# Optimization experiments

Measured on AMD Instinct MI355X. Metric: run time of the kernel, lower is better.

The kernel has to match this reference:

```python
import jax, jax.numpy as jnp
import numpy as np

B, N, DIN, DOUT, H = 4, 2048, 256, 256, 4
HD = DOUT // H
NEG_SLOPE = 0.2


def setup_inputs() -> dict:
    key = jax.random.key(0)
    k1, k2, k3, k4, k5 = jax.random.split(key, 5)
    x = jax.random.normal(k1, (B, N, DIN), dtype=jnp.float32)
    adj = jax.random.randint(k2, (B, N, N), 0, 2).astype(jnp.float32)
    # ensure self-loops so every softmax row has at least one valid entry
    adj = jnp.maximum(adj, jnp.eye(N, dtype=jnp.float32)[None])
    # xavier-uniform-ish scales
    w_bound = float(np.sqrt(6.0 / (DIN + DOUT)))
    a_bound = float(np.sqrt(6.0 / (1 + HD)))
    W = jax.random.uniform(k3, (DOUT, DIN), jnp.float32, -w_bound, w_bound)
    a_src = jax.random.uniform(k4, (H, HD), jnp.float32, -a_bound, a_bound)
    a_dst = jax.random.uniform(k5, (H, HD), jnp.float32, -a_bound, a_bound)
    return {"x": x, "adj": adj, "W": W, "a_src": a_src, "a_dst": a_dst}


def reference(x, adj, W, a_src, a_dst):
    b, n, _ = x.shape
    h = (x @ W.T).reshape(b, n, H, HD)                      # [B,N,H,HD]
    s_src = jnp.einsum('bnhd,hd->bnh', h, a_src)            # [B,N,H]
    s_dst = jnp.einsum('bnhd,hd->bnh', h, a_dst)            # [B,N,H]
    # e[b,i,j,h] = leaky_relu(s_src[b,i,h] + s_dst[b,j,h])
    e = jax.nn.leaky_relu(s_src[:, :, None, :] + s_dst[:, None, :, :], NEG_SLOPE)
    e = jnp.where(adj[..., None] == 0, -jnp.inf, e)         # [B,N,N,H]
    alpha = jax.nn.softmax(e, axis=2)                       # softmax over j (dropout is identity at eval)
    out = jnp.einsum('bijh,bjhd->bihd', alpha, h)           # weighted aggregate
    return out.reshape(b, n, DOUT)
```

## Files before the change

### kernel.cpp

```cpp
#include <hip/hip_runtime.h>
#include <math.h>

#define Bb   4
#define Nn   2048
#define Dd   256
#define Hh   4
#define HDd  64
#define BN   (Bb * Nn)

typedef float v4f __attribute__((ext_vector_type(4)));
typedef short v8s __attribute__((ext_vector_type(8)));

__device__ __forceinline__ unsigned rne_bf16(float f) {
    unsigned u = __float_as_uint(f);
    u += 0x7fffu + ((u >> 16) & 1u);
    return u >> 16;
}

__global__ __launch_bounds__(256, 2) void k_gemm(const float* __restrict__ x,
                                                 const float* __restrict__ W,
                                                 const float* __restrict__ a_src,
                                                 const float* __restrict__ a_dst,
                                                 unsigned short* __restrict__ hbf,
                                                 float* __restrict__ ssrc,
                                                 float* __restrict__ sdst) {
    __shared__ __align__(16) unsigned short xs[2][64 * 72];
    __shared__ __align__(16) unsigned short wsm[2][64 * 72];
    __shared__ float asd[128];

    const int tid = threadIdx.x;
    const int m0 = (int)(blockIdx.x >> 2) * 64;
    const int head = (int)blockIdx.x & 3;
    const int n0 = head * 64;
    const int b = m0 >> 11;
    const int i0loc = m0 & 2047;

    if (tid < 128) {
        int sel = tid >> 6, d = tid & 63;
        asd[tid] = sel ? a_dst[n0 + d] : a_src[n0 + d];
    }

    const int wv = tid >> 6, ln = tid & 63, l15 = ln & 15, l4 = ln >> 4;
    const int mh = wv >> 1, nh = wv & 1;
    const int srow = tid >> 2, kq = (tid & 3) * 16;

    v4f acc[2][2];
#pragma unroll
    for (int g = 0; g < 2; ++g)
#pragma unroll
        for (int t = 0; t < 2; ++t) acc[g][t] = (v4f){0.f, 0.f, 0.f, 0.f};

    for (int st = 0; st < 4; ++st) {
        const int k0 = st * 64;
        __syncthreads();
        {
            float xf[16], wf[16];
            const float* xp = x + (size_t)(m0 + srow) * Dd + k0 + kq;
            const float* wp = W + (size_t)(n0 + srow) * Dd + k0 + kq;
#pragma unroll
            for (int q = 0; q < 4; ++q) {
                *(float4*)&xf[q * 4] = *(const float4*)(xp + q * 4);
                *(float4*)&wf[q * 4] = *(const float4*)(wp + q * 4);
            }
            unsigned xh[8], xl[8], wh[8], wl[8];
#pragma unroll
            for (int j = 0; j < 8; ++j) {
                unsigned h0 = rne_bf16(xf[2 * j]), h1 = rne_bf16(xf[2 * j + 1]);
                float l0 = xf[2 * j] - __uint_as_float(h0 << 16);
                float l1 = xf[2 * j + 1] - __uint_as_float(h1 << 16);
                xh[j] = h0 | (h1 << 16);
                xl[j] = rne_bf16(l0) | (rne_bf16(l1) << 16);
                unsigned g0 = rne_bf16(wf[2 * j]), g1 = rne_bf16(wf[2 * j + 1]);
                float m0f = wf[2 * j] - __uint_as_float(g0 << 16);
                float m1f = wf[2 * j + 1] - __uint_as_float(g1 << 16);
                wh[j] = g0 | (g1 << 16);
                wl[j] = rne_bf16(m0f) | (rne_bf16(m1f) << 16);
            }
            *(uint4*)(xs[0] + srow * 72 + kq)     = make_uint4(xh[0], xh[1], xh[2], xh[3]);
            *(uint4*)(xs[0] + srow * 72 + kq + 8) = make_uint4(xh[4], xh[5], xh[6], xh[7]);
            *(uint4*)(xs[1] + srow * 72 + kq)     = make_uint4(xl[0], xl[1], xl[2], xl[3]);
            *(uint4*)(xs[1] + srow * 72 + kq + 8) = make_uint4(xl[4], xl[5], xl[6], xl[7]);
            *(uint4*)(wsm[0] + srow * 72 + kq)     = make_uint4(wh[0], wh[1], wh[2], wh[3]);
            *(uint4*)(wsm[0] + srow * 72 + kq + 8) = make_uint4(wh[4], wh[5], wh[6], wh[7]);
            *(uint4*)(wsm[1] + srow * 72 + kq)     = make_uint4(wl[0], wl[1], wl[2], wl[3]);
            *(uint4*)(wsm[1] + srow * 72 + kq + 8) = make_uint4(wl[4], wl[5], wl[6], wl[7]);
        }
        __syncthreads();
        {
            v8s ah[2][2], al[2][2], bh_[2][2], bl_[2][2];
#pragma unroll
            for (int g = 0; g < 2; ++g)
#pragma unroll
                for (int kh = 0; kh < 2; ++kh) {
                    int ro = (mh * 32 + g * 16 + l15) * 72 + kh * 32 + l4 * 8;
                    ah[g][kh] = *(const v8s*)(xs[0] + ro);
                    al[g][kh] = *(const v8s*)(xs[1] + ro);
                }
#pragma unroll
            for (int t = 0; t < 2; ++t)
#pragma unroll
                for (int kh = 0; kh < 2; ++kh) {
                    int ro = (nh * 32 + t * 16 + l15) * 72 + kh * 32 + l4 * 8;
                    bh_[t][kh] = *(const v8s*)(wsm[0] + ro);
                    bl_[t][kh] = *(const v8s*)(wsm[1] + ro);
                }
#pragma unroll
            for (int g = 0; g < 2; ++g)
#pragma unroll
                for (int t = 0; t < 2; ++t)
#pragma unroll
                    for (int kh = 0; kh < 2; ++kh) {
                        acc[g][t] = __builtin_amdgcn_mfma_f32_16x16x32_bf16(ah[g][kh], bh_[t][kh], acc[g][t], 0, 0, 0);
                        acc[g][t] = __builtin_amdgcn_mfma_f32_16x16x32_bf16(al[g][kh], bh_[t][kh], acc[g][t], 0, 0, 0);
                        acc[g][t] = __builtin_amdgcn_mfma_f32_16x16x32_bf16(ah[g][kh], bl_[t][kh], acc[g][t], 0, 0, 0);
                    }
        }
    }

    __syncthreads();
    float* T = (float*)&xs[0][0];
#pragma unroll
    for (int g = 0; g < 2; ++g)
#pragma unroll
        for (int t = 0; t < 2; ++t)
#pragma unroll
            for (int r = 0; r < 4; ++r) {
                int d = nh * 32 + t * 16 + l15;
                int m = mh * 32 + g * 16 + l4 * 4 + r;
                T[d * 67 + m] = acc[g][t][r];
            }
    __syncthreads();
    if (tid < 128) {
        int m = tid & 63, sel = tid >> 6;
        float s = 0.f;
#pragma unroll
        for (int d = 0; d < 64; ++d) s += T[d * 67 + m] * asd[sel * 64 + d];
        (sel ? sdst : ssrc)[(size_t)head * BN + (size_t)b * Nn + i0loc + m] = s;
        int dloc = tid >> 1, jh = tid & 1;
        const float* row = T + dloc * 67 + jh * 32;
        unsigned pk[16];
#pragma unroll
        for (int jj = 0; jj < 16; ++jj)
            pk[jj] = rne_bf16(row[jj * 2]) | (rne_bf16(row[jj * 2 + 1]) << 16);
        unsigned short* dst = hbf +
            ((size_t)((b * 64 + (i0loc >> 5) + jh) * 256 + head * HDd + dloc)) * 32;
        uint4* d4 = (uint4*)dst;
        d4[0] = make_uint4(pk[0], pk[1], pk[2], pk[3]);
        d4[1] = make_uint4(pk[4], pk[5], pk[6], pk[7]);
        d4[2] = make_uint4(pk[8], pk[9], pk[10], pk[11]);
        d4[3] = make_uint4(pk[12], pk[13], pk[14], pk[15]);
    }
}

__global__ __launch_bounds__(512, 4) void k_aggr(const unsigned short* __restrict__ hbf,
                                                 const float* __restrict__ adj,
                                                 const float* __restrict__ ssrc,
                                                 const float* __restrict__ sdst,
                                                 float* __restrict__ out) {
    __shared__ __align__(16) unsigned short Aw[2][64 * 72];

    const int tid = threadIdx.x;
    const int bid = (int)blockIdx.x;
    const int hp  = (bid >> 3) & 1;
    const int lin = (bid & 7) | ((bid >> 4) << 3);
    const int b  = lin >> 6;
    const int i0 = (lin & 63) * 32;

    const int gi = tid >> 4, jq = tid & 15;
    const int wv = tid >> 6;
    const int hl = wv >> 2, tl = wv & 3;
    const int ln = tid & 63, l15 = ln & 15, l4 = ln >> 4;

    const float ss0 = ssrc[(size_t)(hp * 2 + 0) * BN + (size_t)b * Nn + i0 + gi];
    const float ss1 = ssrc[(size_t)(hp * 2 + 1) * BN + (size_t)b * Nn + i0 + gi];
    const float* adjr = adj + (size_t)b * Nn * Nn + (size_t)(i0 + gi) * Nn;
    const float* sdr0 = sdst + (size_t)(hp * 2 + 0) * BN + (size_t)b * Nn;
    const float* sdr1 = sdst + (size_t)(hp * 2 + 1) * BN + (size_t)b * Nn;

    const unsigned short* hrow = hbf +
        ((size_t)b * 64 * 256 + (size_t)(hp * 128 + hl * 64 + tl * 16 + l15)) * 32 + l4 * 8;

    const v8s ones = {0x3F80, 0x3F80, 0x3F80, 0x3F80, 0x3F80, 0x3F80, 0x3F80, 0x3F80};

    v4f acc[2], zac[2];
#pragma unroll
    for (int g = 0; g < 2; ++g) {
        acc[g] = (v4f){0.f, 0.f, 0.f, 0.f};
        zac[g] = (v4f){0.f, 0.f, 0.f, 0.f};
    }

    float4 ajv = *(const float4*)(adjr + jq * 4);
    float4 sda = *(const float4*)(sdr0 + jq * 4);
    float4 sdb = *(const float4*)(sdr1 + jq * 4);

    for (int st = 0; st < 32; ++st) {
        {
            const float adjv[4] = {ajv.x, ajv.y, ajv.z, ajv.w};
            const float sa[4] = {sda.x, sda.y, sda.z, sda.w};
            const float sb[4] = {sdb.x, sdb.y, sdb.z, sdb.w};
            unsigned pk0[2], pk1[2];
#pragma unroll
            for (int k = 0; k < 4; ++k) {
                float e0 = ss0 + sa[k];
                float e1 = ss1 + sb[k];
                e0 = fmaxf(e0, 0.2f * e0);
                e1 = fmaxf(e1, 0.2f * e1);
                unsigned u0 = rne_bf16(adjv[k] * __expf(e0));
                unsigned u1 = rne_bf16(adjv[k] * __expf(e1));
                if (k & 1) { pk0[k >> 1] |= u0 << 16; pk1[k >> 1] |= u1 << 16; }
                else       { pk0[k >> 1] = u0;        pk1[k >> 1] = u1; }
            }
            *(uint2*)(Aw[st & 1] + gi * 72 + jq * 4)        = make_uint2(pk0[0], pk0[1]);
            *(uint2*)(Aw[st & 1] + (32 + gi) * 72 + jq * 4) = make_uint2(pk1[0], pk1[1]);
        }
        __syncthreads();
        {
            const int jn = ((st + 1) & 31) * 64;
            ajv = *(const float4*)(adjr + jn + jq * 4);
            sda = *(const float4*)(sdr0 + jn + jq * 4);
            sdb = *(const float4*)(sdr1 + jn + jq * 4);
        }
        {
            const unsigned short* awp = Aw[st & 1];
            v8s b0 = *(const v8s*)(hrow + (size_t)(2 * st + 0) * 8192);
            v8s b1 = *(const v8s*)(hrow + (size_t)(2 * st + 1) * 8192);
            v8s a00 = *(const v8s*)(awp + (hl * 32 + l15) * 72 + l4 * 8);
            v8s a01 = *(const v8s*)(awp + (hl * 32 + l15) * 72 + 32 + l4 * 8);
            v8s a10 = *(const v8s*)(awp + (hl * 32 + 16 + l15) * 72 + l4 * 8);
            v8s a11 = *(const v8s*)(awp + (hl * 32 + 16 + l15) * 72 + 32 + l4 * 8);
            acc[0] = __builtin_amdgcn_mfma_f32_16x16x32_bf16(a00, b0, acc[0], 0, 0, 0);
            acc[0] = __builtin_amdgcn_mfma_f32_16x16x32_bf16(a01, b1, acc[0], 0, 0, 0);
            acc[1] = __builtin_amdgcn_mfma_f32_16x16x32_bf16(a10, b0, acc[1], 0, 0, 0);
            acc[1] = __builtin_amdgcn_mfma_f32_16x16x32_bf16(a11, b1, acc[1], 0, 0, 0);
            zac[0] = __builtin_amdgcn_mfma_f32_16x16x32_bf16(a00, ones, zac[0], 0, 0, 0);
            zac[0] = __builtin_amdgcn_mfma_f32_16x16x32_bf16(a01, ones, zac[0], 0, 0, 0);
            zac[1] = __builtin_amdgcn_mfma_f32_16x16x32_bf16(a10, ones, zac[1], 0, 0, 0);
            zac[1] = __builtin_amdgcn_mfma_f32_16x16x32_bf16(a11, ones, zac[1], 0, 0, 0);
        }
    }

    const int head = hp * 2 + hl;
    const int d = head * HDd + tl * 16 + l15;
#pragma unroll
    for (int g = 0; g < 2; ++g)
#pragma unroll
        for (int r = 0; r < 4; ++r) {
            float zinv = 1.f / zac[g][r];
            int i = i0 + g * 16 + l4 * 4 + r;
            out[((size_t)b * Nn + i) * Dd + d] = acc[g][r] * zinv;
        }
}

extern "C" void kernel_launch(void* const* d_in, const int* in_sizes, int n_in,
                              void* d_out, int out_size, void* d_ws, size_t ws_size,
                              hipStream_t stream) {
    const float* x     = (const float*)d_in[0];
    const float* adj   = (const float*)d_in[1];
    const float* W     = (const float*)d_in[2];
    const float* a_src = (const float*)d_in[3];
    const float* a_dst = (const float*)d_in[4];
    float* out = (float*)d_out;

    unsigned short* hbf = (unsigned short*)d_ws;
    float* ssrc = (float*)(hbf + (size_t)Bb * Nn * Dd);
    float* sdst = ssrc + (size_t)Hh * BN;

    k_gemm<<<dim3(512), dim3(256), 0, stream>>>(x, W, a_src, a_dst, hbf, ssrc, sdst);
    k_aggr<<<dim3(512), dim3(512), 0, stream>>>(hbf, adj, ssrc, sdst, out);
}
```

Before: 154.2 us.

## Generate attention weights directly in MFMA A-fragment registers, drop LDS staging

The aggregation kernel no longer writes bf16 attention weights to shared memory and synchronizes each step. Each wave instead computes its own A fragment in registers from adj/sdst loads laid out to match the MFMA operand, and covers a full head (four 16-column tiles) for 16 rows. Loads are double-buffered by hand across steps, and the block shrinks to 256 threads. This removes the LDS round trip and the barriers. In exchange, adj rows are read by both head waves, so exp work is duplicated per head pair and register pressure goes up.

```diff
diff --git a/kernel.cpp b/kernel.cpp
--- a/kernel.cpp
+++ b/kernel.cpp
@@ -152,13 +152,11 @@
     }
 }
 
-__global__ __launch_bounds__(512, 4) void k_aggr(const unsigned short* __restrict__ hbf,
+__global__ __launch_bounds__(256, 2) void k_aggr(const unsigned short* __restrict__ hbf,
                                                  const float* __restrict__ adj,
                                                  const float* __restrict__ ssrc,
                                                  const float* __restrict__ sdst,
                                                  float* __restrict__ out) {
-    __shared__ __align__(16) unsigned short Aw[2][64 * 72];
-
     const int tid = threadIdx.x;
     const int bid = (int)blockIdx.x;
     const int hp  = (bid >> 3) & 1;
@@ -166,89 +164,112 @@
     const int b  = lin >> 6;
     const int i0 = (lin & 63) * 32;
 
-    const int gi = tid >> 4, jq = tid & 15;
     const int wv = tid >> 6;
-    const int hl = wv >> 2, tl = wv & 3;
+    const int h  = hp * 2 + (wv >> 1);
+    const int isub = wv & 1;
     const int ln = tid & 63, l15 = ln & 15, l4 = ln >> 4;
 
-    const float ss0 = ssrc[(size_t)(hp * 2 + 0) * BN + (size_t)b * Nn + i0 + gi];
-    const float ss1 = ssrc[(size_t)(hp * 2 + 1) * BN + (size_t)b * Nn + i0 + gi];
-    const float* adjr = adj + (size_t)b * Nn * Nn + (size_t)(i0 + gi) * Nn;
-    const float* sdr0 = sdst + (size_t)(hp * 2 + 0) * BN + (size_t)b * Nn;
-    const float* sdr1 = sdst + (size_t)(hp * 2 + 1) * BN + (size_t)b * Nn;
-
-    const unsigned short* hrow = hbf +
-        ((size_t)b * 64 * 256 + (size_t)(hp * 128 + hl * 64 + tl * 16 + l15)) * 32 + l4 * 8;
+    const int irow = i0 + isub * 16 + l15;
+    const float ss = ssrc[(size_t)h * BN + (size_t)b * Nn + irow];
+    const float* adjr = adj  + ((size_t)b * Nn + irow) * Nn + l4 * 8;
+    const float* sdr  = sdst + (size_t)h * BN + (size_t)b * Nn + l4 * 8;
+    const unsigned short* hb0 = hbf +
+        ((size_t)b * 64 * 256 + (size_t)(h * HDd + l15)) * 32 + l4 * 8;
 
     const v8s ones = {0x3F80, 0x3F80, 0x3F80, 0x3F80, 0x3F80, 0x3F80, 0x3F80, 0x3F80};
 
-    v4f acc[2], zac[2];
-#pragma unroll
-    for (int g = 0; g < 2; ++g) {
-        acc[g] = (v4f){0.f, 0.f, 0.f, 0.f};
-        zac[g] = (v4f){0.f, 0.f, 0.f, 0.f};
-    }
-
-    float4 ajv = *(const float4*)(adjr + jq * 4);
-    float4 sda = *(const float4*)(sdr0 + jq * 4);
-    float4 sdb = *(const float4*)(sdr1 + jq * 4);
-
-    for (int st = 0; st < 32; ++st) {
-        {
-            const float adjv[4] = {ajv.x, ajv.y, ajv.z, ajv.w};
-            const float sa[4] = {sda.x, sda.y, sda.z, sda.w};
-            const float sb[4] = {sdb.x, sdb.y, sdb.z, sdb.w};
-            unsigned pk0[2], pk1[2];
-#pragma unroll
-            for (int k = 0; k < 4; ++k) {
-                float e0 = ss0 + sa[k];
-                float e1 = ss1 + sb[k];
-                e0 = fmaxf(e0, 0.2f * e0);
-                e1 = fmaxf(e1, 0.2f * e1);
-                unsigned u0 = rne_bf16(adjv[k] * __expf(e0));
-                unsigned u1 = rne_bf16(adjv[k] * __expf(e1));
-                if (k & 1) { pk0[k >> 1] |= u0 << 16; pk1[k >> 1] |= u1 << 16; }
-                else       { pk0[k >> 1] = u0;        pk1[k >> 1] = u1; }
-            }
-            *(uint2*)(Aw[st & 1] + gi * 72 + jq * 4)        = make_uint2(pk0[0], pk0[1]);
-            *(uint2*)(Aw[st & 1] + (32 + gi) * 72 + jq * 4) = make_uint2(pk1[0], pk1[1]);
-        }
-        __syncthreads();
-        {
-            const int jn = ((st + 1) & 31) * 64;
-            ajv = *(const float4*)(adjr + jn + jq * 4);
-            sda = *(const float4*)(sdr0 + jn + jq * 4);
-            sdb = *(const float4*)(sdr1 + jn + jq * 4);
-        }
-        {
-            const unsigned short* awp = Aw[st & 1];
-            v8s b0 = *(const v8s*)(hrow + (size_t)(2 * st + 0) * 8192);
-            v8s b1 = *(const v8s*)(hrow + (size_t)(2 * st + 1) * 8192);
-            v8s a00 = *(const v8s*)(awp + (hl * 32 + l15) * 72 + l4 * 8);
-            v8s a01 = *(const v8s*)(awp + (hl * 32 + l15) * 72 + 32 + l4 * 8);
-            v8s a10 = *(const v8s*)(awp + (hl * 32 + 16 + l15) * 72 + l4 * 8);
-            v8s a11 = *(const v8s*)(awp + (hl * 32 + 16 + l15) * 72 + 32 + l4 * 8);
-            acc[0] = __builtin_amdgcn_mfma_f32_16x16x32_bf16(a00, b0, acc[0], 0, 0, 0);
-            acc[0] = __builtin_amdgcn_mfma_f32_16x16x32_bf16(a01, b1, acc[0], 0, 0, 0);
-            acc[1] = __builtin_amdgcn_mfma_f32_16x16x32_bf16(a10, b0, acc[1], 0, 0, 0);
-            acc[1] = __builtin_amdgcn_mfma_f32_16x16x32_bf16(a11, b1, acc[1], 0, 0, 0);
-            zac[0] = __builtin_amdgcn_mfma_f32_16x16x32_bf16(a00, ones, zac[0], 0, 0, 0);
-            zac[0] = __builtin_amdgcn_mfma_f32_16x16x32_bf16(a01, ones, zac[0], 0, 0, 0);
-            zac[1] = __builtin_amdgcn_mfma_f32_16x16x32_bf16(a10, ones, zac[1], 0, 0, 0);
-            zac[1] = __builtin_amdgcn_mfma_f32_16x16x32_bf16(a11, ones, zac[1], 0, 0, 0);
-        }
-    }
-
-    const int head = hp * 2 + hl;
-    const int d = head * HDd + tl * 16 + l15;
-#pragma unroll
-    for (int g = 0; g < 2; ++g)
-#pragma unroll
-        for (int r = 0; r < 4; ++r) {
-            float zinv = 1.f / zac[g][r];
-            int i = i0 + g * 16 + l4 * 4 + r;
-            out[((size_t)b * Nn + i) * Dd + d] = acc[g][r] * zinv;
-        }
+    v4f acc[4], zac;
+#pragma unroll
+    for (int t = 0; t < 4; ++t) acc[t] = (v4f){0.f, 0.f, 0.f, 0.f};
+    zac = (v4f){0.f, 0.f, 0.f, 0.f};
+
+    v8s bA[8], bB[8];
+    float4 ajA[4], sdA[4], ajB[4], sdB[4];
+
+#define LOADS(stn, bb, aj_, sd_) do {                                         \
+        const int js_ = (stn) & 31;                                           \
+        const float* ap_ = adjr + js_ * 64;                                   \
+        aj_[0] = *(const float4*)(ap_ + 0);                                   \
+        aj_[1] = *(const float4*)(ap_ + 4);                                   \
+        aj_[2] = *(const float4*)(ap_ + 32);                                  \
+        aj_[3] = *(const float4*)(ap_ + 36);                                  \
+        const float* sp_ = sdr + js_ * 64;                                    \
+        sd_[0] = *(const float4*)(sp_ + 0);                                   \
+        sd_[1] = *(const float4*)(sp_ + 4);                                   \
+        sd_[2] = *(const float4*)(sp_ + 32);                                  \
+        sd_[3] = *(const float4*)(sp_ + 36);                                  \
+        const unsigned short* hq_ = hb0 + (size_t)js_ * 16384;                \
+        bb[0] = *(const v8s*)(hq_ + 0);                                       \
+        bb[1] = *(const v8s*)(hq_ + 8192);                                    \
+        bb[2] = *(const v8s*)(hq_ + 512);                                     \
+        bb[3] = *(const v8s*)(hq_ + 8192 + 512);                              \
+        bb[4] = *(const v8s*)(hq_ + 1024);                                    \
+        bb[5] = *(const v8s*)(hq_ + 8192 + 1024);                             \
+        bb[6] = *(const v8s*)(hq_ + 1536);                                    \
+        bb[7] = *(const v8s*)(hq_ + 8192 + 1536);                             \
+    } while (0)
+
+#define GENW(ssv, sdv, ajv) ({                                                \
+        float e_ = (ssv) + (sdv);                                             \
+        e_ = fmaxf(e_, 0.2f * e_);                                            \
+        (ajv) * __expf(e_);                                                   \
+    })
+
+#define GENFRAG(dst, ajx, ajy, sdx, sdy) do {                                 \
+        float w0_ = GENW(ss, sdx.x, ajx.x);                                   \
+        float w1_ = GENW(ss, sdx.y, ajx.y);                                   \
+        float w2_ = GENW(ss, sdx.z, ajx.z);                                   \
+        float w3_ = GENW(ss, sdx.w, ajx.w);                                   \
+        float w4_ = GENW(ss, sdy.x, ajy.x);                                   \
+        float w5_ = GENW(ss, sdy.y, ajy.y);                                   \
+        float w6_ = GENW(ss, sdy.z, ajy.z);                                   \
+        float w7_ = GENW(ss, sdy.w, ajy.w);                                   \
+        union { v8s v; unsigned u[4]; } P_;                                   \
+        P_.u[0] = rne_bf16(w0_) | (rne_bf16(w1_) << 16);                      \
+        P_.u[1] = rne_bf16(w2_) | (rne_bf16(w3_) << 16);                      \
+        P_.u[2] = rne_bf16(w4_) | (rne_bf16(w5_) << 16);                      \
+        P_.u[3] = rne_bf16(w6_) | (rne_bf16(w7_) << 16);                      \
+        dst = P_.v;                                                           \
+    } while (0)
+
+#define STEP(bb, aj_, sd_) do {                                               \
+        v8s afr0, afr1;                                                       \
+        GENFRAG(afr0, aj_[0], aj_[1], sd_[0], sd_[1]);                        \
+        GENFRAG(afr1, aj_[2], aj_[3], sd_[2], sd_[3]);                        \
+        acc[0] = __builtin_amdgcn_mfma_f32_16x16x32_bf16(afr0, bb[0], acc[0], 0, 0, 0); \
+        acc[1] = __builtin_amdgcn_mfma_f32_16x16x32_bf16(afr0, bb[2], acc[1], 0, 0, 0); \
+        acc[2] = __builtin_amdgcn_mfma_f32_16x16x32_bf16(afr0, bb[4], acc[2], 0, 0, 0); \
+        acc[3] = __builtin_amdgcn_mfma_f32_16x16x32_bf16(afr0, bb[6], acc[3], 0, 0, 0); \
+        zac    = __builtin_amdgcn_mfma_f32_16x16x32_bf16(afr0, ones,  zac,    0, 0, 0); \
+        acc[0] = __builtin_amdgcn_mfma_f32_16x16x32_bf16(afr1, bb[1], acc[0], 0, 0, 0); \
+        acc[1] = __builtin_amdgcn_mfma_f32_16x16x32_bf16(afr1, bb[3], acc[1], 0, 0, 0); \
+        acc[2] = __builtin_amdgcn_mfma_f32_16x16x32_bf16(afr1, bb[5], acc[2], 0, 0, 0); \
+        acc[3] = __builtin_amdgcn_mfma_f32_16x16x32_bf16(afr1, bb[7], acc[3], 0, 0, 0); \
+        zac    = __builtin_amdgcn_mfma_f32_16x16x32_bf16(afr1, ones,  zac,    0, 0, 0); \
+    } while (0)
+
+    LOADS(0, bA, ajA, sdA);
+    for (int st = 0; st < 32; st += 2) {
+        LOADS(st + 1, bB, ajB, sdB);
+        STEP(bA, ajA, sdA);
+        LOADS(st + 2, bA, ajA, sdA);
+        STEP(bB, ajB, sdB);
+    }
+
+#undef LOADS
+#undef GENW
+#undef GENFRAG
+#undef STEP
+
+    float zi[4];
+#pragma unroll
+    for (int r = 0; r < 4; ++r) zi[r] = 1.f / zac[r];
+    float* op = out + ((size_t)b * Nn + i0 + isub * 16 + l4 * 4) * Dd + h * HDd + l15;
+#pragma unroll
+    for (int r = 0; r < 4; ++r)
+#pragma unroll
+        for (int t = 0; t < 4; ++t)
+            op[(size_t)r * Dd + t * 16] = acc[t][r] * zi[r];
 }
 
 extern "C" void kernel_launch(void* const* d_in, const int* in_sizes, int n_in,
@@ -266,5 +287,5 @@
     float* sdst = ssrc + (size_t)Hh * BN;
 
     k_gemm<<<dim3(512), dim3(256), 0, stream>>>(x, W, a_src, a_dst, hbf, ssrc, sdst);
-    k_aggr<<<dim3(512), dim3(512), 0, stream>>>(hbf, adj, ssrc, sdst, out);
-}
+    k_aggr<<<dim3(512), dim3(256), 0, stream>>>(hbf, adj, ssrc, sdst, out);
+}
```

Result: slower. 207.8 us (+34.8%).
